# Kernel tuning notes

Measured on AMD Instinct MI355X. Metric: run time of the kernel, lower is better.

## Reference

```python
import jax, jax.numpy as jnp
import numpy as np

B, H, S, D = 2, 8, 2048, 64
WINDOW = 3            # local_attention_window (default in torch forward)
FRAC = 0.3            # percentage_frac hardcoded in create_window_tensor call
MASK_FILL = -1.0e9


def window_kernel(window, frac):
    # create_window_tensor: [ (1-f)^n ... (1-f)^1, 1, (1-f)^1 ... (1-f)^n ]
    n = (window - 1) // 2
    side = np.array([(1.0 - frac) ** i for i in range(n, 0, -1)], dtype=np.float32)
    vals = np.concatenate([side, np.array([1.0], np.float32), side[::-1]])
    return jnp.asarray(vals)


def setup_inputs() -> dict:
    key = jax.random.key(0)
    kq, kk, kv = jax.random.split(key, 3)
    queries = jax.random.normal(kq, (B, H, S, D), jnp.float32)
    keys = jax.random.normal(kk, (B, H, S, D), jnp.float32)
    values = jax.random.normal(kv, (B, H, S, D), jnp.float32)
    # causal mask: True positions are filled with -1e9 (masked_fill semantics)
    mask = jnp.triu(jnp.ones((S, S), dtype=bool), 1)[None, None]  # [1,1,S,S]
    # linear_bias: nn.Parameter(torch.zeros(Sk)) created inside forward
    beta = jnp.zeros((S,), jnp.float32)
    return {"queries": queries, "keys": keys, "values": values,
            "beta": beta, "mask": mask}


def reference(queries, keys, values, beta, mask):
    d = keys.shape[-1]
    # scores = Q K^T / sqrt(d)
    scores = jnp.einsum("bhqd,bhkd->bhqk", queries, keys) / jnp.sqrt(
        jnp.asarray(d, queries.dtype))
    scores = jnp.where(mask, jnp.asarray(MASK_FILL, scores.dtype), scores)
    # include_local_attention=True, local_attention_dim_vertical=False:
    # the torch code transposes, conv2d with a [1,W] kernel along the last
    # axis, transposes back -> 1D cross-correlation along the QUERY axis.
    # Kernel is symmetric so correlation == convolution. Zero padding.
    kern = window_kernel(WINDOW, FRAC)
    p = (WINDOW - 1) // 2
    xp = jnp.pad(scores, ((0, 0), (0, 0), (p, p), (0, 0)))
    Sq = scores.shape[2]
    scores = sum(kern[i] * jax.lax.dynamic_slice_in_dim(xp, i, Sq, axis=2)
                 for i in range(WINDOW))
    # linear_bias=True: add zero-initialized per-key-position bias
    scores = scores + beta  # broadcasts over last dim [Sk]
    weights = jax.nn.softmax(scores, axis=-1)
    return jnp.einsum("bhqk,bhkd->bhqd", weights, values)
```

## Files before the change

### kernel.cpp

```cpp
#include <hip/hip_runtime.h>


typedef short bf16x8 __attribute__((ext_vector_type(8)));
typedef float f32x4  __attribute__((ext_vector_type(4)));

constexpr int S_ = 2048;
constexpr int D_ = 64;
constexpr int KSTR = 72;
constexpr float LOG2E = 1.44269504088896341f;
constexpr float KSC = 0.125f * LOG2E;

__device__ __forceinline__ unsigned pk2(float lo, float hi) {
    union { float f; unsigned u; } a, b;
    a.f = lo; b.f = hi;
    return __builtin_amdgcn_perm(b.u + 0x8000u, a.u + 0x8000u, 0x07060302u);
}

__global__ __launch_bounds__(256, 3)
void attn5(const float* __restrict__ Q, const float* __restrict__ K,
           const float* __restrict__ V, const float* __restrict__ beta,
           float* __restrict__ out)
{
    __shared__ __align__(16) unsigned short smem[18432];

    const int bid = blockIdx.x;
    const int bh = bid & 15;
    const int qt = 31 - (bid >> 4);
    const int q0 = qt << 6;
    const int nt = qt + 1;

    const float* Qh = Q + bh * (S_ * D_);
    const float* Kh = K + bh * (S_ * D_);
    const float* Vh = V + bh * (S_ * D_);

    const int t = threadIdx.x, lane = t & 63;
    const int wv = t >> 6, kh = wv & 1, qh = wv >> 1;
    const int n_l = lane & 15, qd = lane >> 4;

    const int rk = t >> 2, c0 = (t & 3) << 1;
    const int kw0 = rk * KSTR + ((c0 + (rk >> 3)) & 7) * 8;
    const int kw1 = rk * KSTR + ((c0 + 1 + (rk >> 3)) & 7) * 8;
    const int k2 = (t & 31) << 1, dg = t >> 5;
    const int vw = (dg << 3) * KSTR + ((((k2 >> 3) + dg) & 7) << 3) + (k2 & 7);

    int aoff[2][2];
    {
        const int krb = (kh << 5) + ((n_l >> 2) << 3) + (n_l & 3);
        #pragma unroll
        for (int mb = 0; mb < 2; ++mb) {
            const int krow = krb + (mb << 2);
            #pragma unroll
            for (int h = 0; h < 2; ++h)
                aoff[mb][h] = krow * KSTR + ((((h << 2) + qd) + (krow >> 3)) & 7) * 8;
        }
    }
    int voff[4];
    #pragma unroll
    for (int mb = 0; mb < 4; ++mb) {
        const int d = (mb << 4) + n_l;
        voff[mb] = d * KSTR + ((((kh << 2) + qd) + (d >> 3)) & 7) * 8;
    }

    float kr[16], vr[16];
    const float* kgp = Kh + rk * D_ + (c0 << 3);
    const float* vgp = Vh + k2 * D_ + (dg << 3);
    #pragma unroll
    for (int i = 0; i < 4; ++i) *(float4*)&kr[4 * i] = *(const float4*)(kgp + 4 * i);
    *(float4*)&vr[0]  = *(const float4*)(vgp);
    *(float4*)&vr[4]  = *(const float4*)(vgp + 4);
    *(float4*)&vr[8]  = *(const float4*)(vgp + D_);
    *(float4*)&vr[12] = *(const float4*)(vgp + D_ + 4);

    unsigned short* Qs = &smem[4608];
    {
        const int r = t >> 2, d16 = (t & 3) << 4;
        const int q = q0 + r;
        const float wp = (q > 0) ? 0.7f : 0.0f;
        const float wn = (q + 1 < S_) ? 0.7f : 0.0f;
        const float* qc = Qh + q * D_ + d16;
        const float* qp = qc - ((q > 0) ? D_ : 0);
        const float* qn = qc + ((q + 1 < S_) ? D_ : 0);
        unsigned pkd[8];
        #pragma unroll
        for (int i = 0; i < 4; ++i) {
            float4 c4 = *(const float4*)(qc + 4 * i);
            float4 p4 = *(const float4*)(qp + 4 * i);
            float4 n4 = *(const float4*)(qn + 4 * i);
            float e0 = fmaf(wn, n4.x, fmaf(wp, p4.x, c4.x));
            float e1 = fmaf(wn, n4.y, fmaf(wp, p4.y, c4.y));
            float e2 = fmaf(wn, n4.z, fmaf(wp, p4.z, c4.z));
            float e3 = fmaf(wn, n4.w, fmaf(wp, p4.w, c4.w));
            pkd[2 * i]     = pk2(e0, e1);
            pkd[2 * i + 1] = pk2(e2, e3);
        }
        *(uint4*)&Qs[r * KSTR + d16]     = make_uint4(pkd[0], pkd[1], pkd[2], pkd[3]);
        *(uint4*)&Qs[r * KSTR + d16 + 8] = make_uint4(pkd[4], pkd[5], pkd[6], pkd[7]);
    }
    __syncthreads();

    bf16x8 qb[2][2];
    #pragma unroll
    for (int ng = 0; ng < 2; ++ng) {
        const int row = (qh << 5) + (ng << 4) + n_l;
        qb[ng][0] = *(const bf16x8*)&Qs[row * KSTR + (qd << 3)];
        qb[ng][1] = *(const bf16x8*)&Qs[row * KSTR + 32 + (qd << 3)];
    }

    {
        unsigned pkd[8];
        #pragma unroll
        for (int i = 0; i < 8; ++i) pkd[i] = pk2(kr[2 * i], kr[2 * i + 1]);
        *(uint4*)&smem[kw0] = make_uint4(pkd[0], pkd[1], pkd[2], pkd[3]);
        *(uint4*)&smem[kw1] = make_uint4(pkd[4], pkd[5], pkd[6], pkd[7]);
        #pragma unroll
        for (int i = 0; i < 8; ++i)
            *(unsigned*)&smem[9216 + vw + i * KSTR] = pk2(vr[i], vr[8 + i]);
    }
    __syncthreads();

    if (nt > 1) {
        #pragma unroll
        for (int i = 0; i < 4; ++i) *(float4*)&kr[4 * i] = *(const float4*)(kgp + 4096 + 4 * i);
        *(float4*)&vr[0]  = *(const float4*)(vgp + 4096);
        *(float4*)&vr[4]  = *(const float4*)(vgp + 4100);
        *(float4*)&vr[8]  = *(const float4*)(vgp + 4096 + D_);
        *(float4*)&vr[12] = *(const float4*)(vgp + 4100 + D_);
    }

    f32x4 o[4][2];
    float l[2] = {0.0f, 0.0f};
    #pragma unroll
    for (int mb = 0; mb < 4; ++mb)
        #pragma unroll
        for (int ng = 0; ng < 2; ++ng) o[mb][ng] = (f32x4){0, 0, 0, 0};

    const int kbase = (kh << 5) + (qd << 3);
    const float* bp = beta + kbase;

    for (int it = 0; it < nt; ++it) {
        const int kcb = (it & 1) ? 4608 : 0;
        const int vcb = (it & 1) ? 13824 : 9216;

        if (it + 1 < nt) {
            const int kwb = (it & 1) ? 0 : 4608;
            const int vwb = (it & 1) ? 9216 : 13824;
            unsigned pkd[8];
            #pragma unroll
            for (int i = 0; i < 8; ++i) pkd[i] = pk2(kr[2 * i], kr[2 * i + 1]);
            *(uint4*)&smem[kwb + kw0] = make_uint4(pkd[0], pkd[1], pkd[2], pkd[3]);
            *(uint4*)&smem[kwb + kw1] = make_uint4(pkd[4], pkd[5], pkd[6], pkd[7]);
            #pragma unroll
            for (int i = 0; i < 8; ++i)
                *(unsigned*)&smem[vwb + vw + i * KSTR] = pk2(vr[i], vr[8 + i]);
        }
        __syncthreads();

        if (it + 2 < nt) {
            const float* kp = kgp + (it + 2) * 4096;
            const float* vp = vgp + (it + 2) * 4096;
            #pragma unroll
            for (int i = 0; i < 4; ++i) *(float4*)&kr[4 * i] = *(const float4*)(kp + 4 * i);
            *(float4*)&vr[0]  = *(const float4*)(vp);
            *(float4*)&vr[4]  = *(const float4*)(vp + 4);
            *(float4*)&vr[8]  = *(const float4*)(vp + D_);
            *(float4*)&vr[12] = *(const float4*)(vp + D_ + 4);
        }
        const float4 bt0 = *(const float4*)(bp + (it << 6));
        const float4 bt1 = *(const float4*)(bp + (it << 6) + 4);

        bf16x8 ka[2][2], va[4];
        #pragma unroll
        for (int mb = 0; mb < 2; ++mb)
            #pragma unroll
            for (int h = 0; h < 2; ++h)
                ka[mb][h] = *(const bf16x8*)&smem[kcb + aoff[mb][h]];
        #pragma unroll
        for (int mb = 0; mb < 4; ++mb) va[mb] = *(const bf16x8*)&smem[vcb + voff[mb]];

        const f32x4 zz = {0, 0, 0, 0};
        f32x4 acc[2][2];
        #pragma unroll
        for (int mb = 0; mb < 2; ++mb)
            #pragma unroll
            for (int ng = 0; ng < 2; ++ng) {
                f32x4 a = __builtin_amdgcn_mfma_f32_16x16x32_bf16(ka[mb][0], qb[ng][0], zz, 0, 0, 0);
                acc[mb][ng] = __builtin_amdgcn_mfma_f32_16x16x32_bf16(ka[mb][1], qb[ng][1], a, 0, 0, 0);
            }

        const float btf[8] = {bt0.x * LOG2E, bt0.y * LOG2E, bt0.z * LOG2E, bt0.w * LOG2E,
                              bt1.x * LOG2E, bt1.y * LOG2E, bt1.z * LOG2E, bt1.w * LOG2E};
        const bool dm = (it == qt);
        const int kk = (it << 6) + kbase;

        union { unsigned u[4]; bf16x8 v; } pf[2];
        #pragma unroll
        for (int ng = 0; ng < 2; ++ng) {
            const int qr = q0 + (qh << 5) + (ng << 4) + n_l;
            float p[8];
            float lacc = 0.0f;
            #pragma unroll
            for (int j = 0; j < 8; ++j) {
                const int mb = j >> 2, r = j & 3;
                float sv = fmaf(acc[mb][ng][r], KSC, btf[j]);
                if (dm) {
                    const int key = kk + j;
                    if (!((key < qr) || (qr == 0 && key == 0))) sv = -1.0e30f;
                }
                p[j] = __builtin_amdgcn_exp2f(sv);
                lacc += p[j];
            }
            l[ng] += lacc;
            pf[ng].u[0] = pk2(p[0], p[1]);
            pf[ng].u[1] = pk2(p[2], p[3]);
            pf[ng].u[2] = pk2(p[4], p[5]);
            pf[ng].u[3] = pk2(p[6], p[7]);
        }

        #pragma unroll
        for (int mb = 0; mb < 4; ++mb)
            #pragma unroll
            for (int ng = 0; ng < 2; ++ng)
                o[mb][ng] = __builtin_amdgcn_mfma_f32_16x16x32_bf16(va[mb], pf[ng].v, o[mb][ng], 0, 0, 0);

        __syncthreads();
    }

    #pragma unroll
    for (int ng = 0; ng < 2; ++ng) {
        l[ng] += __shfl_xor(l[ng], 16);
        l[ng] += __shfl_xor(l[ng], 32);
    }
    float* opub = (float*)smem;
    float* lred = opub + 4352;
    if (kh == 0) {
        #pragma unroll
        for (int ng = 0; ng < 2; ++ng) {
            const int row = (qh << 5) + (ng << 4) + n_l;
            #pragma unroll
            for (int mb = 0; mb < 4; ++mb)
                *(float4*)&opub[row * 68 + (mb << 4) + (qd << 2)] =
                    make_float4(o[mb][ng][0], o[mb][ng][1], o[mb][ng][2], o[mb][ng][3]);
            if (qd == 0) lred[row] = l[ng];
        }
    }
    __syncthreads();
    if (kh == 1) {
        #pragma unroll
        for (int ng = 0; ng < 2; ++ng) {
            const int row = (qh << 5) + (ng << 4) + n_l;
            const float inv = 1.0f / (l[ng] + lred[row]);
            float* op = out + ((size_t)bh * S_ + q0 + row) * D_ + (qd << 2);
            #pragma unroll
            for (int mb = 0; mb < 4; ++mb) {
                float4 pv = *(float4*)&opub[row * 68 + (mb << 4) + (qd << 2)];
                *(float4*)(op + (mb << 4)) =
                    make_float4((o[mb][ng][0] + pv.x) * inv, (o[mb][ng][1] + pv.y) * inv,
                                (o[mb][ng][2] + pv.z) * inv, (o[mb][ng][3] + pv.w) * inv);
            }
        }
    }
}

extern "C" void kernel_launch(void* const* d_in, const int* in_sizes, int n_in,
                              void* d_out, int out_size, void* d_ws, size_t ws_size,
                              hipStream_t stream) {
    const float* Q    = (const float*)d_in[0];
    const float* K    = (const float*)d_in[1];
    const float* V    = (const float*)d_in[2];
    const float* beta = (const float*)d_in[3];
    float* out = (float*)d_out;

    attn5<<<dim3(512), dim3(256), 0, stream>>>(Q, K, V, beta, out);
}
```

Before: 134.0 us.

## Pre-convert K/V to bf16 workspace, load MFMA operands directly from global, pair causal tiles

Adds two pre-pass kernels: one converts K to bf16 and one converts V to a transposed bf16 layout, both written into the workspace. The attention kernel then loads MFMA fragments straight from global memory into registers with a two-stage register double buffer, with no LDS staging and no per-tile barriers. Each block handles two query tiles, j and 31-j, to balance the causal workload, and the grid drops to 256 blocks. The costs are two extra launches and the extra memory traffic of the pre-pass, and the global loads for MFMA fragments are less coalesced than the old LDS path.

```diff
diff --git a/kernel.cpp b/kernel.cpp
--- a/kernel.cpp
+++ b/kernel.cpp
@@ -6,7 +6,6 @@
 
 constexpr int S_ = 2048;
 constexpr int D_ = 64;
-constexpr int KSTR = 72;
 constexpr float LOG2E = 1.44269504088896341f;
 constexpr float KSC = 0.125f * LOG2E;
 
@@ -16,246 +15,226 @@
     return __builtin_amdgcn_perm(b.u + 0x8000u, a.u + 0x8000u, 0x07060302u);
 }
 
-__global__ __launch_bounds__(256, 3)
-void attn5(const float* __restrict__ Q, const float* __restrict__ K,
-           const float* __restrict__ V, const float* __restrict__ beta,
+__global__ __launch_bounds__(256)
+void cvt_k(const float* __restrict__ K, unsigned short* __restrict__ Kbf)
+{
+    const size_t i = ((size_t)blockIdx.x * 256 + threadIdx.x) * 8;
+    float4 a = *(const float4*)(K + i);
+    float4 b = *(const float4*)(K + i + 4);
+    *(uint4*)(Kbf + i) = make_uint4(pk2(a.x, a.y), pk2(a.z, a.w),
+                                    pk2(b.x, b.y), pk2(b.z, b.w));
+}
+
+__global__ __launch_bounds__(256)
+void cvt_v(const float* __restrict__ V, unsigned short* __restrict__ Vt)
+{
+    __shared__ float T[64][65];
+    const int k0 = blockIdx.x << 6;
+    const int hd = blockIdx.y;
+    const int t = threadIdx.x;
+    {
+        const int ky = t >> 2, dc = (t & 3) << 4;
+        const float* vp = V + (((size_t)hd * S_) + k0 + ky) * D_ + dc;
+        #pragma unroll
+        for (int i = 0; i < 4; ++i) {
+            float4 v4 = *(const float4*)(vp + 4 * i);
+            T[ky][dc + 4 * i + 0] = v4.x;
+            T[ky][dc + 4 * i + 1] = v4.y;
+            T[ky][dc + 4 * i + 2] = v4.z;
+            T[ky][dc + 4 * i + 3] = v4.w;
+        }
+    }
+    __syncthreads();
+    {
+        const int d = t >> 2, kc = (t & 3) << 4;
+        unsigned w[8];
+        #pragma unroll
+        for (int j = 0; j < 8; ++j)
+            w[j] = pk2(T[kc + 2 * j][d], T[kc + 2 * j + 1][d]);
+        unsigned short* op = Vt + ((size_t)hd * D_ + d) * S_ + k0 + kc;
+        *(uint4*)(op)     = make_uint4(w[0], w[1], w[2], w[3]);
+        *(uint4*)(op + 8) = make_uint4(w[4], w[5], w[6], w[7]);
+    }
+}
+
+__global__ __launch_bounds__(256, 2)
+void attn6(const float* __restrict__ Q, const float* __restrict__ beta,
+           const unsigned short* __restrict__ Kbf, const unsigned short* __restrict__ Vt,
            float* __restrict__ out)
 {
-    __shared__ __align__(16) unsigned short smem[18432];
+    __shared__ float opub[2][32][68];
+    __shared__ float lred[2][32];
 
     const int bid = blockIdx.x;
-    const int bh = bid & 15;
-    const int qt = 31 - (bid >> 4);
-    const int q0 = qt << 6;
-    const int nt = qt + 1;
-
-    const float* Qh = Q + bh * (S_ * D_);
-    const float* Kh = K + bh * (S_ * D_);
-    const float* Vh = V + bh * (S_ * D_);
+    const int hd = bid & 15;
+    const int pr = bid >> 4;
+
+    const float* Qh = Q + (size_t)hd * S_ * D_;
+    const unsigned short* Kh = Kbf + (size_t)hd * S_ * D_;
+    const unsigned short* Vh = Vt + (size_t)hd * D_ * S_;
 
     const int t = threadIdx.x, lane = t & 63;
-    const int wv = t >> 6, kh = wv & 1, qh = wv >> 1;
+    const int wv = t >> 6, kh = wv & 1, sg = wv >> 1;
     const int n_l = lane & 15, qd = lane >> 4;
-
-    const int rk = t >> 2, c0 = (t & 3) << 1;
-    const int kw0 = rk * KSTR + ((c0 + (rk >> 3)) & 7) * 8;
-    const int kw1 = rk * KSTR + ((c0 + 1 + (rk >> 3)) & 7) * 8;
-    const int k2 = (t & 31) << 1, dg = t >> 5;
-    const int vw = (dg << 3) * KSTR + ((((k2 >> 3) + dg) & 7) << 3) + (k2 & 7);
-
-    int aoff[2][2];
-    {
-        const int krb = (kh << 5) + ((n_l >> 2) << 3) + (n_l & 3);
-        #pragma unroll
-        for (int mb = 0; mb < 2; ++mb) {
-            const int krow = krb + (mb << 2);
-            #pragma unroll
-            for (int h = 0; h < 2; ++h)
-                aoff[mb][h] = krow * KSTR + ((((h << 2) + qd) + (krow >> 3)) & 7) * 8;
-        }
-    }
-    int voff[4];
+    const int qdo = qd << 3;
+
+    int krow[2];
+    krow[0] = (kh << 5) + ((n_l >> 2) << 3) + (n_l & 3);
+    krow[1] = krow[0] + 4;
+    int dmb[4];
     #pragma unroll
-    for (int mb = 0; mb < 4; ++mb) {
-        const int d = (mb << 4) + n_l;
-        voff[mb] = d * KSTR + ((((kh << 2) + qd) + (d >> 3)) & 7) * 8;
-    }
-
-    float kr[16], vr[16];
-    const float* kgp = Kh + rk * D_ + (c0 << 3);
-    const float* vgp = Vh + k2 * D_ + (dg << 3);
-    #pragma unroll
-    for (int i = 0; i < 4; ++i) *(float4*)&kr[4 * i] = *(const float4*)(kgp + 4 * i);
-    *(float4*)&vr[0]  = *(const float4*)(vgp);
-    *(float4*)&vr[4]  = *(const float4*)(vgp + 4);
-    *(float4*)&vr[8]  = *(const float4*)(vgp + D_);
-    *(float4*)&vr[12] = *(const float4*)(vgp + D_ + 4);
-
-    unsigned short* Qs = &smem[4608];
-    {
-        const int r = t >> 2, d16 = (t & 3) << 4;
-        const int q = q0 + r;
-        const float wp = (q > 0) ? 0.7f : 0.0f;
-        const float wn = (q + 1 < S_) ? 0.7f : 0.0f;
-        const float* qc = Qh + q * D_ + d16;
-        const float* qp = qc - ((q > 0) ? D_ : 0);
-        const float* qn = qc + ((q + 1 < S_) ? D_ : 0);
-        unsigned pkd[8];
-        #pragma unroll
-        for (int i = 0; i < 4; ++i) {
-            float4 c4 = *(const float4*)(qc + 4 * i);
-            float4 p4 = *(const float4*)(qp + 4 * i);
-            float4 n4 = *(const float4*)(qn + 4 * i);
-            float e0 = fmaf(wn, n4.x, fmaf(wp, p4.x, c4.x));
-            float e1 = fmaf(wn, n4.y, fmaf(wp, p4.y, c4.y));
-            float e2 = fmaf(wn, n4.z, fmaf(wp, p4.z, c4.z));
-            float e3 = fmaf(wn, n4.w, fmaf(wp, p4.w, c4.w));
-            pkd[2 * i]     = pk2(e0, e1);
-            pkd[2 * i + 1] = pk2(e2, e3);
-        }
-        *(uint4*)&Qs[r * KSTR + d16]     = make_uint4(pkd[0], pkd[1], pkd[2], pkd[3]);
-        *(uint4*)&Qs[r * KSTR + d16 + 8] = make_uint4(pkd[4], pkd[5], pkd[6], pkd[7]);
-    }
-    __syncthreads();
-
-    bf16x8 qb[2][2];
-    #pragma unroll
-    for (int ng = 0; ng < 2; ++ng) {
-        const int row = (qh << 5) + (ng << 4) + n_l;
-        qb[ng][0] = *(const bf16x8*)&Qs[row * KSTR + (qd << 3)];
-        qb[ng][1] = *(const bf16x8*)&Qs[row * KSTR + 32 + (qd << 3)];
-    }
-
-    {
-        unsigned pkd[8];
-        #pragma unroll
-        for (int i = 0; i < 8; ++i) pkd[i] = pk2(kr[2 * i], kr[2 * i + 1]);
-        *(uint4*)&smem[kw0] = make_uint4(pkd[0], pkd[1], pkd[2], pkd[3]);
-        *(uint4*)&smem[kw1] = make_uint4(pkd[4], pkd[5], pkd[6], pkd[7]);
-        #pragma unroll
-        for (int i = 0; i < 8; ++i)
-            *(unsigned*)&smem[9216 + vw + i * KSTR] = pk2(vr[i], vr[8 + i]);
-    }
-    __syncthreads();
-
-    if (nt > 1) {
-        #pragma unroll
-        for (int i = 0; i < 4; ++i) *(float4*)&kr[4 * i] = *(const float4*)(kgp + 4096 + 4 * i);
-        *(float4*)&vr[0]  = *(const float4*)(vgp + 4096);
-        *(float4*)&vr[4]  = *(const float4*)(vgp + 4100);
-        *(float4*)&vr[8]  = *(const float4*)(vgp + 4096 + D_);
-        *(float4*)&vr[12] = *(const float4*)(vgp + 4100 + D_);
-    }
-
-    f32x4 o[4][2];
-    float l[2] = {0.0f, 0.0f};
-    #pragma unroll
-    for (int mb = 0; mb < 4; ++mb)
-        #pragma unroll
-        for (int ng = 0; ng < 2; ++ng) o[mb][ng] = (f32x4){0, 0, 0, 0};
-
-    const int kbase = (kh << 5) + (qd << 3);
-    const float* bp = beta + kbase;
-
-    for (int it = 0; it < nt; ++it) {
-        const int kcb = (it & 1) ? 4608 : 0;
-        const int vcb = (it & 1) ? 13824 : 9216;
-
-        if (it + 1 < nt) {
-            const int kwb = (it & 1) ? 0 : 4608;
-            const int vwb = (it & 1) ? 9216 : 13824;
-            unsigned pkd[8];
-            #pragma unroll
-            for (int i = 0; i < 8; ++i) pkd[i] = pk2(kr[2 * i], kr[2 * i + 1]);
-            *(uint4*)&smem[kwb + kw0] = make_uint4(pkd[0], pkd[1], pkd[2], pkd[3]);
-            *(uint4*)&smem[kwb + kw1] = make_uint4(pkd[4], pkd[5], pkd[6], pkd[7]);
-            #pragma unroll
-            for (int i = 0; i < 8; ++i)
-                *(unsigned*)&smem[vwb + vw + i * KSTR] = pk2(vr[i], vr[8 + i]);
+    for (int mb = 0; mb < 4; ++mb) dmb[mb] = (mb << 4) + n_l;
+    const int kvo = (kh << 5) + qdo;
+
+    for (int p = 0; p < 2; ++p) {
+        const int j = p ? (31 - pr) : pr;
+        const int q0 = j << 6;
+        const int nt = j + 1;
+        const int qbase = q0 + (sg << 5);
+
+        auto ld = [&](int tile, bf16x8 (&ka)[2][2], bf16x8 (&vb)[4], float (&bt)[8]) {
+            const unsigned short* kp = Kh + (size_t)(tile << 6) * D_;
+            #pragma unroll
+            for (int mb = 0; mb < 2; ++mb)
+                #pragma unroll
+                for (int hh = 0; hh < 2; ++hh)
+                    ka[mb][hh] = *(const bf16x8*)(kp + krow[mb] * D_ + (hh << 5) + qdo);
+            const unsigned short* vp = Vh + (tile << 6) + kvo;
+            #pragma unroll
+            for (int mb = 0; mb < 4; ++mb)
+                vb[mb] = *(const bf16x8*)(vp + (size_t)dmb[mb] * S_);
+            const float* bp = beta + (tile << 6) + kvo;
+            float4 b0 = *(const float4*)(bp);
+            float4 b1 = *(const float4*)(bp + 4);
+            bt[0] = b0.x * LOG2E; bt[1] = b0.y * LOG2E;
+            bt[2] = b0.z * LOG2E; bt[3] = b0.w * LOG2E;
+            bt[4] = b1.x * LOG2E; bt[5] = b1.y * LOG2E;
+            bt[6] = b1.z * LOG2E; bt[7] = b1.w * LOG2E;
+        };
+
+        bf16x8 kaA[2][2], vbA[4]; float btA[8];
+        bf16x8 kaB[2][2], vbB[4]; float btB[8];
+        ld(0, kaA, vbA, btA);
+
+        bf16x8 qb[2][2];
+        #pragma unroll
+        for (int ng = 0; ng < 2; ++ng) {
+            const int q = qbase + (ng << 4) + n_l;
+            const float wp = (q > 0) ? 0.7f : 0.0f;
+            const float wn = (q + 1 < S_) ? 0.7f : 0.0f;
+            const float* qc = Qh + (size_t)q * D_;
+            const float* qpp = qc - ((q > 0) ? D_ : 0);
+            const float* qnn = qc + ((q + 1 < S_) ? D_ : 0);
+            #pragma unroll
+            for (int hh = 0; hh < 2; ++hh) {
+                const int d0 = (hh << 5) + qdo;
+                float4 c0 = *(const float4*)(qc + d0),  c1 = *(const float4*)(qc + d0 + 4);
+                float4 p0 = *(const float4*)(qpp + d0), p1 = *(const float4*)(qpp + d0 + 4);
+                float4 n0 = *(const float4*)(qnn + d0), n1 = *(const float4*)(qnn + d0 + 4);
+                float e0 = fmaf(wn, n0.x, fmaf(wp, p0.x, c0.x));
+                float e1 = fmaf(wn, n0.y, fmaf(wp, p0.y, c0.y));
+                float e2 = fmaf(wn, n0.z, fmaf(wp, p0.z, c0.z));
+                float e3 = fmaf(wn, n0.w, fmaf(wp, p0.w, c0.w));
+                float e4 = fmaf(wn, n1.x, fmaf(wp, p1.x, c1.x));
+                float e5 = fmaf(wn, n1.y, fmaf(wp, p1.y, c1.y));
+                float e6 = fmaf(wn, n1.z, fmaf(wp, p1.z, c1.z));
+                float e7 = fmaf(wn, n1.w, fmaf(wp, p1.w, c1.w));
+                union { unsigned u[4]; bf16x8 v; } qu;
+                qu.u[0] = pk2(e0, e1); qu.u[1] = pk2(e2, e3);
+                qu.u[2] = pk2(e4, e5); qu.u[3] = pk2(e6, e7);
+                qb[ng][hh] = qu.v;
+            }
+        }
+
+        f32x4 o[4][2];
+        float l[2] = {0.0f, 0.0f};
+        #pragma unroll
+        for (int mb = 0; mb < 4; ++mb)
+            #pragma unroll
+            for (int ng = 0; ng < 2; ++ng) o[mb][ng] = (f32x4){0, 0, 0, 0};
+
+        auto comp = [&](int tile, bf16x8 (&ka)[2][2], bf16x8 (&vb)[4], float (&bt)[8]) {
+            const f32x4 zz = {0, 0, 0, 0};
+            f32x4 acc[2][2];
+            #pragma unroll
+            for (int mb = 0; mb < 2; ++mb)
+                #pragma unroll
+                for (int ng = 0; ng < 2; ++ng) {
+                    f32x4 a = __builtin_amdgcn_mfma_f32_16x16x32_bf16(ka[mb][0], qb[ng][0], zz, 0, 0, 0);
+                    acc[mb][ng] = __builtin_amdgcn_mfma_f32_16x16x32_bf16(ka[mb][1], qb[ng][1], a, 0, 0, 0);
+                }
+            const bool dm = (tile == nt - 1);
+            const int kk = (tile << 6) + kvo;
+            union { unsigned u[4]; bf16x8 v; } pf[2];
+            #pragma unroll
+            for (int ng = 0; ng < 2; ++ng) {
+                const int qr = qbase + (ng << 4) + n_l;
+                float pv[8];
+                float la = 0.0f;
+                #pragma unroll
+                for (int jj = 0; jj < 8; ++jj) {
+                    const int mb = jj >> 2, r = jj & 3;
+                    float sv = fmaf(acc[mb][ng][r], KSC, bt[jj]);
+                    if (dm) {
+                        const int key = kk + jj;
+                        if (!((key < qr) || (qr == 0 && key == 0))) sv = -1.0e30f;
+                    }
+                    pv[jj] = __builtin_amdgcn_exp2f(sv);
+                    la += pv[jj];
+                }
+                l[ng] += la;
+                pf[ng].u[0] = pk2(pv[0], pv[1]);
+                pf[ng].u[1] = pk2(pv[2], pv[3]);
+                pf[ng].u[2] = pk2(pv[4], pv[5]);
+                pf[ng].u[3] = pk2(pv[6], pv[7]);
+            }
+            #pragma unroll
+            for (int mb = 0; mb < 4; ++mb)
+                #pragma unroll
+                for (int ng = 0; ng < 2; ++ng)
+                    o[mb][ng] = __builtin_amdgcn_mfma_f32_16x16x32_bf16(vb[mb], pf[ng].v, o[mb][ng], 0, 0, 0);
+        };
+
+        int it = 0;
+        for (; it + 2 <= nt; it += 2) {
+            ld(it + 1, kaB, vbB, btB);
+            comp(it, kaA, vbA, btA);
+            if (it + 2 < nt) ld(it + 2, kaA, vbA, btA);
+            comp(it + 1, kaB, vbB, btB);
+        }
+        if (it < nt) comp(it, kaA, vbA, btA);
+
+        #pragma unroll
+        for (int ng = 0; ng < 2; ++ng) {
+            l[ng] += __shfl_xor(l[ng], 16);
+            l[ng] += __shfl_xor(l[ng], 32);
         }
         __syncthreads();
-
-        if (it + 2 < nt) {
-            const float* kp = kgp + (it + 2) * 4096;
-            const float* vp = vgp + (it + 2) * 4096;
-            #pragma unroll
-            for (int i = 0; i < 4; ++i) *(float4*)&kr[4 * i] = *(const float4*)(kp + 4 * i);
-            *(float4*)&vr[0]  = *(const float4*)(vp);
-            *(float4*)&vr[4]  = *(const float4*)(vp + 4);
-            *(float4*)&vr[8]  = *(const float4*)(vp + D_);
-            *(float4*)&vr[12] = *(const float4*)(vp + D_ + 4);
-        }
-        const float4 bt0 = *(const float4*)(bp + (it << 6));
-        const float4 bt1 = *(const float4*)(bp + (it << 6) + 4);
-
-        bf16x8 ka[2][2], va[4];
-        #pragma unroll
-        for (int mb = 0; mb < 2; ++mb)
-            #pragma unroll
-            for (int h = 0; h < 2; ++h)
-                ka[mb][h] = *(const bf16x8*)&smem[kcb + aoff[mb][h]];
-        #pragma unroll
-        for (int mb = 0; mb < 4; ++mb) va[mb] = *(const bf16x8*)&smem[vcb + voff[mb]];
-
-        const f32x4 zz = {0, 0, 0, 0};
-        f32x4 acc[2][2];
-        #pragma unroll
-        for (int mb = 0; mb < 2; ++mb)
+        if (kh == 0) {
             #pragma unroll
             for (int ng = 0; ng < 2; ++ng) {
-                f32x4 a = __builtin_amdgcn_mfma_f32_16x16x32_bf16(ka[mb][0], qb[ng][0], zz, 0, 0, 0);
-                acc[mb][ng] = __builtin_amdgcn_mfma_f32_16x16x32_bf16(ka[mb][1], qb[ng][1], a, 0, 0, 0);
-            }
-
-        const float btf[8] = {bt0.x * LOG2E, bt0.y * LOG2E, bt0.z * LOG2E, bt0.w * LOG2E,
-                              bt1.x * LOG2E, bt1.y * LOG2E, bt1.z * LOG2E, bt1.w * LOG2E};
-        const bool dm = (it == qt);
-        const int kk = (it << 6) + kbase;
-
-        union { unsigned u[4]; bf16x8 v; } pf[2];
-        #pragma unroll
-        for (int ng = 0; ng < 2; ++ng) {
-            const int qr = q0 + (qh << 5) + (ng << 4) + n_l;
-            float p[8];
-            float lacc = 0.0f;
-            #pragma unroll
-            for (int j = 0; j < 8; ++j) {
-                const int mb = j >> 2, r = j & 3;
-                float sv = fmaf(acc[mb][ng][r], KSC, btf[j]);
-                if (dm) {
-                    const int key = kk + j;
-                    if (!((key < qr) || (qr == 0 && key == 0))) sv = -1.0e30f;
+                const int row = (ng << 4) + n_l;
+                #pragma unroll
+                for (int mb = 0; mb < 4; ++mb)
+                    *(float4*)&opub[sg][row][(mb << 4) + (qd << 2)] =
+                        make_float4(o[mb][ng][0], o[mb][ng][1], o[mb][ng][2], o[mb][ng][3]);
+                if (qd == 0) lred[sg][row] = l[ng];
+            }
+        }
+        __syncthreads();
+        if (kh == 1) {
+            #pragma unroll
+            for (int ng = 0; ng < 2; ++ng) {
+                const int row = (ng << 4) + n_l;
+                const float inv = 1.0f / (l[ng] + lred[sg][row]);
+                float* op = out + ((size_t)hd * S_ + qbase + row) * D_ + (qd << 2);
+                #pragma unroll
+                for (int mb = 0; mb < 4; ++mb) {
+                    float4 pv = *(float4*)&opub[sg][row][(mb << 4) + (qd << 2)];
+                    *(float4*)(op + (mb << 4)) =
+                        make_float4((o[mb][ng][0] + pv.x) * inv, (o[mb][ng][1] + pv.y) * inv,
+                                    (o[mb][ng][2] + pv.z) * inv, (o[mb][ng][3] + pv.w) * inv);
                 }
-                p[j] = __builtin_amdgcn_exp2f(sv);
-                lacc += p[j];
-            }
-            l[ng] += lacc;
-            pf[ng].u[0] = pk2(p[0], p[1]);
-            pf[ng].u[1] = pk2(p[2], p[3]);
-            pf[ng].u[2] = pk2(p[4], p[5]);
-            pf[ng].u[3] = pk2(p[6], p[7]);
-        }
-
-        #pragma unroll
-        for (int mb = 0; mb < 4; ++mb)
-            #pragma unroll
-            for (int ng = 0; ng < 2; ++ng)
-                o[mb][ng] = __builtin_amdgcn_mfma_f32_16x16x32_bf16(va[mb], pf[ng].v, o[mb][ng], 0, 0, 0);
-
-        __syncthreads();
-    }
-
-    #pragma unroll
-    for (int ng = 0; ng < 2; ++ng) {
-        l[ng] += __shfl_xor(l[ng], 16);
-        l[ng] += __shfl_xor(l[ng], 32);
-    }
-    float* opub = (float*)smem;
-    float* lred = opub + 4352;
-    if (kh == 0) {
-        #pragma unroll
-        for (int ng = 0; ng < 2; ++ng) {
-            const int row = (qh << 5) + (ng << 4) + n_l;
-            #pragma unroll
-            for (int mb = 0; mb < 4; ++mb)
-                *(float4*)&opub[row * 68 + (mb << 4) + (qd << 2)] =
-                    make_float4(o[mb][ng][0], o[mb][ng][1], o[mb][ng][2], o[mb][ng][3]);
-            if (qd == 0) lred[row] = l[ng];
-        }
-    }
-    __syncthreads();
-    if (kh == 1) {
-        #pragma unroll
-        for (int ng = 0; ng < 2; ++ng) {
-            const int row = (qh << 5) + (ng << 4) + n_l;
-            const float inv = 1.0f / (l[ng] + lred[row]);
-            float* op = out + ((size_t)bh * S_ + q0 + row) * D_ + (qd << 2);
-            #pragma unroll
-            for (int mb = 0; mb < 4; ++mb) {
-                float4 pv = *(float4*)&opub[row * 68 + (mb << 4) + (qd << 2)];
-                *(float4*)(op + (mb << 4)) =
-                    make_float4((o[mb][ng][0] + pv.x) * inv, (o[mb][ng][1] + pv.y) * inv,
-                                (o[mb][ng][2] + pv.z) * inv, (o[mb][ng][3] + pv.w) * inv);
             }
         }
     }
@@ -270,5 +249,10 @@
     const float* beta = (const float*)d_in[3];
     float* out = (float*)d_out;
 
-    attn5<<<dim3(512), dim3(256), 0, stream>>>(Q, K, V, beta, out);
-}
+    unsigned short* Kbf = (unsigned short*)d_ws;
+    unsigned short* Vt  = Kbf + (size_t)16 * S_ * D_;
+
+    cvt_k<<<dim3(1024), 256, 0, stream>>>(K, Kbf);
+    cvt_v<<<dim3(32, 16), 256, 0, stream>>>(V, Vt);
+    attn6<<<dim3(256), 256, 0, stream>>>(Q, beta, Kbf, Vt, out);
+}
```

After: 128.2 us. 4.3% less time.
